# Optimization experiments

Hardware: AMD Instinct MI355X
Metric: run time of the kernel (lower is better)

Reference implementation:

```python
import jax, jax.numpy as jnp
import numpy as np

# dims: batch, seq, d_model, heads, experts, expert hidden, top-k
B, S, D, H, E, F, K = 8, 512, 768, 12, 8, 3072, 2
DH = D // H
TAU = 1.0  # routing temperature
EPS = 1e-5


def _ln(x, g, b):
    mu = jnp.mean(x, axis=-1, keepdims=True)
    var = jnp.var(x, axis=-1, keepdims=True)
    return (x - mu) * jax.lax.rsqrt(var + EPS) * g + b


def setup_inputs() -> dict:
    key = jax.random.key(0)
    ks = jax.random.split(key, 12)
    sd = 1.0 / np.sqrt(D)
    sf = 1.0 / np.sqrt(F)
    return {
        "x": jax.random.normal(ks[0], (B, S, D), jnp.float32),
        "wq": jax.random.normal(ks[1], (D, D), jnp.float32) * sd,
        "wk": jax.random.normal(ks[2], (D, D), jnp.float32) * sd,
        "wv": jax.random.normal(ks[3], (D, D), jnp.float32) * sd,
        "wo": jax.random.normal(ks[4], (D, D), jnp.float32) * sd,
        "ln1_g": jnp.ones((D,), jnp.float32),
        "ln1_b": jnp.zeros((D,), jnp.float32),
        "ln2_g": jnp.ones((D,), jnp.float32),
        "ln2_b": jnp.zeros((D,), jnp.float32),
        "gate_w": jax.random.normal(ks[5], (D, E), jnp.float32) * sd,
        "gate_b": jnp.zeros((E,), jnp.float32),
        "bias_e": jnp.zeros((E,), jnp.float32),  # bias_param: per-expert routing bias (selection only)
        "w1": jax.random.normal(ks[6], (E, D, F), jnp.float32) * sd,
        "b1": jnp.zeros((E, F), jnp.float32),
        "w2": jax.random.normal(ks[7], (E, F, D), jnp.float32) * sf,
        "b2": jnp.zeros((E, D), jnp.float32),
    }


def reference(x, wq, wk, wv, wo, ln1_g, ln1_b, ln2_g, ln2_b,
              gate_w, gate_b, bias_e, w1, b1, w2, b2):
    # --- pre-LN multi-head self-attention + residual ---
    h = _ln(x, ln1_g, ln1_b)
    q = (h @ wq).reshape(B, S, H, DH)
    k = (h @ wk).reshape(B, S, H, DH)
    v = (h @ wv).reshape(B, S, H, DH)
    scores = jnp.einsum("bqhd,bkhd->bhqk", q, k) / np.sqrt(DH).astype(np.float32)
    attn = jax.nn.softmax(scores, axis=-1)
    o = jnp.einsum("bhqk,bkhd->bqhd", attn, v).reshape(B, S, D) @ wo
    x = x + o

    # --- pre-LN top-k MoE + residual ---
    h = _ln(x, ln2_g, ln2_b).reshape(B * S, D)          # [T, D]
    logits = (h @ gate_w + gate_b) / TAU                # [T, E]
    sel_scores = logits + bias_e                        # bias used for selection only
    _, idx = jax.lax.top_k(sel_scores, K)               # [T, K]
    topk_logits = jnp.take_along_axis(logits, idx, axis=-1)
    gates = jax.nn.softmax(topk_logits, axis=-1)        # [T, K]
    # sparse combine weights [T, E]
    cw = jnp.zeros((B * S, E), x.dtype).at[jnp.arange(B * S)[:, None], idx].set(gates)
    mid = jax.nn.gelu(jnp.einsum("td,edf->tef", h, w1) + b1)   # [T, E, F]
    eout = jnp.einsum("tef,efd->ted", mid, w2) + b2            # [T, E, D]
    y = jnp.einsum("ted,te->td", eout, cw).reshape(B, S, D)
    return x + y
```

## Files before the change

kernel.cpp:

```cpp
#include <hip/hip_runtime.h>
#include <hip/hip_bf16.h>

using bf16 = __hip_bfloat16;

constexpr int NB = 8, NS = 512, ND = 768, NH = 12, NE = 8, NF = 3072, NT = 4096;
constexpr int HG = 4;
constexpr int NG = NH / HG;
constexpr int GW = HG * 64;
constexpr int FQ = 768;
constexpr int NP = NF / FQ;

typedef __attribute__((ext_vector_type(8))) short v8s;
typedef __attribute__((ext_vector_type(4))) float v4f;

__device__ __forceinline__ short f2bf(float v) {
    bf16 t = __float2bfloat16(v);
    return *reinterpret_cast<short*>(&t);
}
__device__ __forceinline__ float bf2f(short s) {
    bf16 t = *reinterpret_cast<bf16*>(&s);
    return __bfloat162float(t);
}

template <typename TOUT>
__launch_bounds__(256)
__global__ void ln_kernel(const float* __restrict__ x, const float* __restrict__ g,
                          const float* __restrict__ b, TOUT* __restrict__ out) {
    const int t = blockIdx.x;
    const int tid = threadIdx.x;
    const float* xr = x + (size_t)t * ND;
    float v0 = xr[tid], v1 = xr[tid + 256], v2 = xr[tid + 512];
    float s = v0 + v1 + v2;
    float ss = v0 * v0 + v1 * v1 + v2 * v2;
#pragma unroll
    for (int off = 32; off >= 1; off >>= 1) {
        s += __shfl_xor(s, off);
        ss += __shfl_xor(ss, off);
    }
    __shared__ float rs[4], rss[4];
    const int wv = tid >> 6, ln = tid & 63;
    if (ln == 0) { rs[wv] = s; rss[wv] = ss; }
    __syncthreads();
    float S = rs[0] + rs[1] + rs[2] + rs[3];
    float SS = rss[0] + rss[1] + rss[2] + rss[3];
    float mu = S * (1.0f / ND);
    float var = SS * (1.0f / ND) - mu * mu;
    float r = rsqrtf(fmaxf(var, 0.f) + 1e-5f);
    TOUT* orow = out + (size_t)t * ND;
    float o0 = (v0 - mu) * r * g[tid]       + b[tid];
    float o1 = (v1 - mu) * r * g[tid + 256] + b[tid + 256];
    float o2 = (v2 - mu) * r * g[tid + 512] + b[tid + 512];
    if constexpr (sizeof(TOUT) == 2) {
        orow[tid] = __float2bfloat16(o0);
        orow[tid + 256] = __float2bfloat16(o1);
        orow[tid + 512] = __float2bfloat16(o2);
    } else {
        orow[tid] = o0; orow[tid + 256] = o1; orow[tid + 512] = o2;
    }
}

__device__ __forceinline__ void gemm3_core(const float* __restrict__ A, int lda,
                                           const float* __restrict__ Bsrc, int ldb,
                                           int Kd, int m0, v4f acc[4],
                                           short* Ah, short* Al, short* Bh, short* Bl) {
    const int tid = threadIdx.x, lane = tid & 63, wv = tid >> 6;
    const int qd = lane >> 4, l16 = lane & 15;
    const int ar = tid >> 2, ac = (tid & 3) * 8;
    const int bn = tid & 63, bk = (tid >> 6) * 8;
    const float* Arow = A + (size_t)(m0 + ar) * lda;
    for (int k0 = 0; k0 < Kd; k0 += 32) {
        {
            const float* asrc = Arow + k0 + ac;
            v8s ah, al;
#pragma unroll
            for (int j = 0; j < 8; j++) {
                float vv = asrc[j];
                short hi = f2bf(vv);
                ah[j] = hi;
                al[j] = f2bf(vv - bf2f(hi));
            }
            *(v8s*)&Ah[ar * 40 + ac] = ah;
            *(v8s*)&Al[ar * 40 + ac] = al;
        }
        {
            const float* bsrc = Bsrc + (size_t)(k0 + bk) * ldb + bn;
            v8s bh_, bl_;
#pragma unroll
            for (int j = 0; j < 8; j++) {
                float vv = bsrc[(size_t)j * ldb];
                short hi = f2bf(vv);
                bh_[j] = hi;
                bl_[j] = f2bf(vv - bf2f(hi));
            }
            *(v8s*)&Bh[bn * 40 + bk] = bh_;
            *(v8s*)&Bl[bn * 40 + bk] = bl_;
        }
        __syncthreads();
        v8s bhf = *(const v8s*)&Bh[(wv * 16 + l16) * 40 + qd * 8];
        v8s blf = *(const v8s*)&Bl[(wv * 16 + l16) * 40 + qd * 8];
#pragma unroll
        for (int t = 0; t < 4; t++) {
            v8s ahf = *(const v8s*)&Ah[(t * 16 + l16) * 40 + qd * 8];
            v8s alf = *(const v8s*)&Al[(t * 16 + l16) * 40 + qd * 8];
            acc[t] = __builtin_amdgcn_mfma_f32_16x16x32_bf16(ahf, bhf, acc[t], 0, 0, 0);
            acc[t] = __builtin_amdgcn_mfma_f32_16x16x32_bf16(ahf, blf, acc[t], 0, 0, 0);
            acc[t] = __builtin_amdgcn_mfma_f32_16x16x32_bf16(alf, bhf, acc[t], 0, 0, 0);
        }
        __syncthreads();
    }
}

template <int RES_MODE>
__launch_bounds__(256)
__global__ void sgemm3(const float* __restrict__ A, int lda, const float* __restrict__ Bw,
                       int ldb, int bcol0, const float* __restrict__ Res,
                       float* __restrict__ C, int ldc, int Kd) {
    __shared__ short Ah[64 * 40], Al[64 * 40], Bh[64 * 40], Bl[64 * 40];
    const int m0 = blockIdx.x * 64, n0 = blockIdx.y * 64;
    v4f acc[4] = {};
    gemm3_core(A, lda, Bw + bcol0 + n0, ldb, Kd, m0, acc, Ah, Al, Bh, Bl);
    const int tid = threadIdx.x, lane = tid & 63, wv = tid >> 6;
    const int qd = lane >> 4, l16 = lane & 15;
    const int c = n0 + wv * 16 + l16;
#pragma unroll
    for (int t = 0; t < 4; t++)
#pragma unroll
        for (int rg = 0; rg < 4; rg++) {
            const int r = m0 + t * 16 + qd * 4 + rg;
            size_t ci = (size_t)r * ldc + c;
            if (RES_MODE == 0) C[ci] = acc[t][rg];
            else if (RES_MODE == 1) C[ci] = Res[ci] + acc[t][rg];
            else C[ci] += acc[t][rg];
        }
}

__launch_bounds__(256)
__global__ void qkv3(const float* __restrict__ h, const float* __restrict__ wq,
                     const float* __restrict__ wk, const float* __restrict__ wv,
                     int bcol0, float* __restrict__ qo, float* __restrict__ ko,
                     float* __restrict__ vo) {
    __shared__ short Ah[64 * 40], Al[64 * 40], Bh[64 * 40], Bl[64 * 40];
    const int m0 = blockIdx.x * 64;
    const int ysel = blockIdx.y >> 2, ny = blockIdx.y & 3;
    const int n0 = ny * 64;
    const float* Bw = (ysel == 0) ? wq : (ysel == 1) ? wk : wv;
    float* C = (ysel == 0) ? qo : (ysel == 1) ? ko : vo;
    v4f acc[4] = {};
    gemm3_core(h, ND, Bw + bcol0 + n0, ND, ND, m0, acc, Ah, Al, Bh, Bl);
    const int tid = threadIdx.x, lane = tid & 63, wv_ = tid >> 6;
    const int qd = lane >> 4, l16 = lane & 15;
    const int c = n0 + wv_ * 16 + l16;
#pragma unroll
    for (int t = 0; t < 4; t++)
#pragma unroll
        for (int rg = 0; rg < 4; rg++) {
            const int r = m0 + t * 16 + qd * 4 + rg;
            C[(size_t)r * GW + c] = acc[t][rg];
        }
}

__launch_bounds__(256)
__global__ void attn_kernel(const float* __restrict__ q, const float* __restrict__ k,
                            const float* __restrict__ v, float* __restrict__ o) {
    __shared__ float qs[64][68];
    __shared__ float kp[64][68];
    __shared__ float vs[64][68];
    const int qt = blockIdx.x, hl = blockIdx.y, b = blockIdx.z;
    const int tid = threadIdx.x, tx = tid & 15, ty = tid >> 4;
    const int hc = hl * 64;
    {
        const v4f* q4 = (const v4f*)(q + ((size_t)b * NS + qt * 64) * GW + hc);
#pragma unroll
        for (int i = 0; i < 4; i++) {
            int idx = tid + 256 * i;
            int r = idx >> 4, c4 = idx & 15;
            *(v4f*)&qs[r][c4 * 4] = q4[(size_t)r * (GW / 4) + c4];
        }
    }
    float oa[4][4] = {};
    float mi[4], li[4], al[4];
#pragma unroll
    for (int i = 0; i < 4; i++) { mi[i] = -1.0e30f; li[i] = 0.f; }
    for (int kt = 0; kt < NS / 64; kt++) {
        __syncthreads();
        {
            const v4f* k4 = (const v4f*)(k + ((size_t)b * NS + kt * 64) * GW + hc);
            const v4f* v4 = (const v4f*)(v + ((size_t)b * NS + kt * 64) * GW + hc);
#pragma unroll
            for (int i = 0; i < 4; i++) {
                int idx = tid + 256 * i;
                int r = idx >> 4, c4 = idx & 15;
                *(v4f*)&kp[r][c4 * 4] = k4[(size_t)r * (GW / 4) + c4];
                *(v4f*)&vs[r][c4 * 4] = v4[(size_t)r * (GW / 4) + c4];
            }
        }
        __syncthreads();
        float s[4][4] = {};
#pragma unroll
        for (int d0 = 0; d0 < 64; d0 += 4) {
            v4f av[4], bv[4];
#pragma unroll
            for (int i = 0; i < 4; i++) av[i] = *(const v4f*)&qs[ty + 16 * i][d0];
#pragma unroll
            for (int j = 0; j < 4; j++) bv[j] = *(const v4f*)&kp[tx + 16 * j][d0];
#pragma unroll
            for (int dd = 0; dd < 4; dd++)
#pragma unroll
                for (int i = 0; i < 4; i++)
#pragma unroll
                    for (int j = 0; j < 4; j++) s[i][j] += av[i][dd] * bv[j][dd];
        }
#pragma unroll
        for (int i = 0; i < 4; i++) {
#pragma unroll
            for (int j = 0; j < 4; j++) s[i][j] *= 0.125f;
            float mt = fmaxf(fmaxf(s[i][0], s[i][1]), fmaxf(s[i][2], s[i][3]));
#pragma unroll
            for (int off = 1; off < 16; off <<= 1) mt = fmaxf(mt, __shfl_xor(mt, off));
            float mn = fmaxf(mi[i], mt);
            al[i] = __expf(mi[i] - mn);
            mi[i] = mn;
            float rsum = 0.f;
#pragma unroll
            for (int j = 0; j < 4; j++) {
                s[i][j] = __expf(s[i][j] - mn);
                rsum += s[i][j];
            }
#pragma unroll
            for (int off = 1; off < 16; off <<= 1) rsum += __shfl_xor(rsum, off);
            li[i] = li[i] * al[i] + rsum;
        }
        __syncthreads();
#pragma unroll
        for (int i = 0; i < 4; i++)
#pragma unroll
            for (int j = 0; j < 4; j++) {
                kp[ty + 16 * i][tx + 16 * j] = s[i][j];
                oa[i][j] *= al[i];
            }
        __syncthreads();
#pragma unroll
        for (int d0 = 0; d0 < 64; d0 += 4) {
            v4f av[4];
#pragma unroll
            for (int i = 0; i < 4; i++) av[i] = *(const v4f*)&kp[ty + 16 * i][d0];
#pragma unroll
            for (int dd = 0; dd < 4; dd++) {
                float bb[4];
#pragma unroll
                for (int j = 0; j < 4; j++) bb[j] = vs[d0 + dd][tx + 16 * j];
#pragma unroll
                for (int i = 0; i < 4; i++)
#pragma unroll
                    for (int j = 0; j < 4; j++) oa[i][j] += av[i][dd] * bb[j];
            }
        }
    }
#pragma unroll
    for (int i = 0; i < 4; i++) {
        float inv = 1.0f / li[i];
#pragma unroll
        for (int j = 0; j < 4; j++)
            o[((size_t)b * NS + qt * 64 + ty + 16 * i) * GW + hc + tx + 16 * j] = oa[i][j] * inv;
    }
}

__launch_bounds__(256)
__global__ void route_kernel(const float* __restrict__ x1, const float* __restrict__ lg,
                             const float* __restrict__ lb, const float* __restrict__ gw,
                             const float* __restrict__ gb, const float* __restrict__ be,
                             int* __restrict__ cnt, int* __restrict__ list,
                             float* __restrict__ gates) {
    const int lane = threadIdx.x & 63;
    const int t = blockIdx.x * 4 + (threadIdx.x >> 6);
    if (t >= NT) return;
    const float* xr = x1 + (size_t)t * ND;
    float xv[12];
    float s = 0.f, ss = 0.f;
#pragma unroll
    for (int i = 0; i < 12; i++) {
        xv[i] = xr[i * 64 + lane];
        s += xv[i];
        ss += xv[i] * xv[i];
    }
#pragma unroll
    for (int off = 32; off >= 1; off >>= 1) {
        s += __shfl_xor(s, off);
        ss += __shfl_xor(ss, off);
    }
    float mu = s * (1.0f / ND);
    float var = ss * (1.0f / ND) - mu * mu;
    float r = rsqrtf(fmaxf(var, 0.f) + 1e-5f);
    float le[NE];
#pragma unroll
    for (int e = 0; e < NE; e++) le[e] = 0.f;
#pragma unroll
    for (int i = 0; i < 12; i++) {
        int d = i * 64 + lane;
        float hn = (xv[i] - mu) * r * lg[d] + lb[d];
#pragma unroll
        for (int e = 0; e < NE; e++) le[e] += hn * gw[d * NE + e];
    }
#pragma unroll
    for (int off = 1; off < 64; off <<= 1)
#pragma unroll
        for (int e = 0; e < NE; e++) le[e] += __shfl_xor(le[e], off);
    float sel[NE];
#pragma unroll
    for (int e = 0; e < NE; e++) {
        le[e] += gb[e];
        sel[e] = le[e] + be[e];
    }
    int i1 = 0;
#pragma unroll
    for (int e = 1; e < NE; e++) if (sel[e] > sel[i1]) i1 = e;
    int i2 = (i1 == 0) ? 1 : 0;
#pragma unroll
    for (int e = 0; e < NE; e++) if (e != i1 && sel[e] > sel[i2]) i2 = e;
    float l1 = le[i1], l2 = le[i2];
    float m = fmaxf(l1, l2);
    float e1 = __expf(l1 - m), e2 = __expf(l2 - m);
    float inv = 1.0f / (e1 + e2);
    if (lane == 0) {
        gates[t * 2 + 0] = e1 * inv;
        gates[t * 2 + 1] = e2 * inv;
        int p1 = atomicAdd(&cnt[i1], 1);
        if (p1 < NT) list[i1 * NT + p1] = t * 2 + 0;
        int p2 = atomicAdd(&cnt[i2], 1);
        if (p2 < NT) list[i2 * NT + p2] = t * 2 + 1;
    }
}

__launch_bounds__(256)
__global__ void moe_gemm1(const bf16* __restrict__ h2, const float* __restrict__ w1,
                          const float* __restrict__ b1, const int* __restrict__ cnt,
                          const int* __restrict__ list, bf16* __restrict__ mid, int fcol0) {
    const int e = blockIdx.x >> 6, tile = blockIdx.x & 63;
    const int n = min(cnt[e], NT);
    const int r0 = tile * 64;
    if (r0 >= n) return;
    const int f0 = blockIdx.y * 64;
    __shared__ int ent[64];
    __shared__ short As[64 * 40];
    __shared__ short Bs[64 * 40];
    const int tid = threadIdx.x;
    const int lane = tid & 63, wv = tid >> 6;
    const int qd = lane >> 4, l16 = lane & 15;
    if (tid < 64) {
        int en = (r0 + tid < n) ? list[e * NT + r0 + tid] : -1;
        if (en < 0 || en >= 2 * NT) en = -1;
        ent[tid] = en;
    }
    __syncthreads();
    v4f acc[4] = {};
    const float* w1e = w1 + (size_t)e * ND * NF + fcol0 + f0;
    const int ar = tid >> 2, ac = (tid & 3) * 8;
    const int bn = tid & 63, bk = (tid >> 6) * 8;
    const int aen = ent[ar];
    for (int k0 = 0; k0 < ND; k0 += 32) {
        v8s av = {};
        if (aen >= 0)
            av = *(const v8s*)((const short*)h2 + (size_t)(aen >> 1) * ND + k0 + ac);
        *(v8s*)&As[ar * 40 + ac] = av;
        {
            const float* src = w1e + (size_t)(k0 + bk) * NF + bn;
            v8s bv;
#pragma unroll
            for (int j = 0; j < 8; j++) bv[j] = f2bf(src[(size_t)j * NF]);
            *(v8s*)&Bs[bn * 40 + bk] = bv;
        }
        __syncthreads();
        v8s bfrag = *(const v8s*)&Bs[(wv * 16 + l16) * 40 + qd * 8];
#pragma unroll
        for (int t = 0; t < 4; t++) {
            v8s afrag = *(const v8s*)&As[(t * 16 + l16) * 40 + qd * 8];
            acc[t] = __builtin_amdgcn_mfma_f32_16x16x32_bf16(afrag, bfrag, acc[t], 0, 0, 0);
        }
        __syncthreads();
    }
    const int col = wv * 16 + l16;
    const float bias = b1[e * NF + fcol0 + f0 + col];
#pragma unroll
    for (int t = 0; t < 4; t++) {
#pragma unroll
        for (int rg = 0; rg < 4; rg++) {
            int en = ent[t * 16 + qd * 4 + rg];
            if (en < 0) continue;
            float xv = acc[t][rg] + bias;
            float th = tanhf(0.7978845608028654f * (xv + 0.044715f * xv * xv * xv));
            mid[((size_t)((en & 1) * NT) + (en >> 1)) * FQ + f0 + col] =
                __float2bfloat16(0.5f * xv * (1.0f + th));
        }
    }
}

__launch_bounds__(256)
__global__ void moe_gemm2(const bf16* __restrict__ mid, const float* __restrict__ w2,
                          const float* __restrict__ b2, const int* __restrict__ cnt,
                          const int* __restrict__ list, const float* __restrict__ gates,
                          float* __restrict__ x1, int fcol0, int add_b2) {
    const int e = blockIdx.x >> 6, tile = blockIdx.x & 63;
    const int n = min(cnt[e], NT);
    const int r0 = tile * 64;
    if (r0 >= n) return;
    const int d0 = blockIdx.y * 64;
    __shared__ int ent[64];
    __shared__ short As[64 * 40];
    __shared__ short Bs[64 * 40];
    const int tid = threadIdx.x;
    const int lane = tid & 63, wv = tid >> 6;
    const int qd = lane >> 4, l16 = lane & 15;
    if (tid < 64) {
        int en = (r0 + tid < n) ? list[e * NT + r0 + tid] : -1;
        if (en < 0 || en >= 2 * NT) en = -1;
        ent[tid] = en;
    }
    __syncthreads();
    v4f acc[4] = {};
    const float* w2e = w2 + (size_t)e * NF * ND + d0;
    const int ar = tid >> 2, ac = (tid & 3) * 8;
    const int bn = tid & 63, bk = (tid >> 6) * 8;
    const int aen = ent[ar];
    for (int k0 = 0; k0 < FQ; k0 += 32) {
        v8s av = {};
        if (aen >= 0)
            av = *(const v8s*)((const short*)mid +
                               ((size_t)((aen & 1) * NT) + (aen >> 1)) * FQ + k0 + ac);
        *(v8s*)&As[ar * 40 + ac] = av;
        {
            const float* src = w2e + (size_t)(fcol0 + k0 + bk) * ND + bn;
            v8s bv;
#pragma unroll
            for (int j = 0; j < 8; j++) bv[j] = f2bf(src[(size_t)j * ND]);
            *(v8s*)&Bs[bn * 40 + bk] = bv;
        }
        __syncthreads();
        v8s bfrag = *(const v8s*)&Bs[(wv * 16 + l16) * 40 + qd * 8];
#pragma unroll
        for (int t = 0; t < 4; t++) {
            v8s afrag = *(const v8s*)&As[(t * 16 + l16) * 40 + qd * 8];
            acc[t] = __builtin_amdgcn_mfma_f32_16x16x32_bf16(afrag, bfrag, acc[t], 0, 0, 0);
        }
        __syncthreads();
    }
    const int col = wv * 16 + l16;
    const float bias = add_b2 ? b2[e * ND + d0 + col] : 0.f;
#pragma unroll
    for (int t = 0; t < 4; t++) {
#pragma unroll
        for (int rg = 0; rg < 4; rg++) {
            int en = ent[t * 16 + qd * 4 + rg];
            if (en < 0) continue;
            float g = gates[en];
            atomicAdd(&x1[(size_t)(en >> 1) * ND + d0 + col], g * (acc[t][rg] + bias));
        }
    }
}

__launch_bounds__(256)
__global__ void final_kernel(const float* __restrict__ x1, float* __restrict__ out) {
    int i = blockIdx.x * 256 + threadIdx.x;
    out[i] = x1[i];
}

extern "C" void kernel_launch(void* const* d_in, const int* in_sizes, int n_in,
                              void* d_out, int out_size, void* d_ws, size_t ws_size,
                              hipStream_t stream) {
    const float* x    = (const float*)d_in[0];
    const float* wq   = (const float*)d_in[1];
    const float* wk   = (const float*)d_in[2];
    const float* wvp  = (const float*)d_in[3];
    const float* wo   = (const float*)d_in[4];
    const float* ln1g = (const float*)d_in[5];
    const float* ln1b = (const float*)d_in[6];
    const float* ln2g = (const float*)d_in[7];
    const float* ln2b = (const float*)d_in[8];
    const float* gw   = (const float*)d_in[9];
    const float* gb   = (const float*)d_in[10];
    const float* be   = (const float*)d_in[11];
    const float* w1   = (const float*)d_in[12];
    const float* b1   = (const float*)d_in[13];
    const float* w2   = (const float*)d_in[14];
    const float* b2   = (const float*)d_in[15];
    float* out = (float*)d_out;

    const size_t TDn = (size_t)NT * ND;
    const size_t TGn = (size_t)NT * GW;
    float* W = (float*)d_ws;
    int*   cnt   = (int*)W;
    int*   list  = cnt + NE;
    float* gates = (float*)(list + NE * NT);
    float* x1 = W + 41216;
    float* h  = x1 + TDn;
    float* R0 = h + TDn;
    float* q  = R0;
    float* k  = R0 + TGn;
    float* v  = R0 + 2 * TGn;
    float* og = R0 + 3 * TGn;
    bf16*  h2  = (bf16*)h;
    bf16*  mid = (bf16*)R0;

    hipMemsetAsync(cnt, 0, NE * sizeof(int), stream);

    ln_kernel<float><<<NT, 256, 0, stream>>>(x, ln1g, ln1b, h);
    for (int g = 0; g < NG; g++) {
        qkv3<<<dim3(NT / 64, 12), 256, 0, stream>>>(h, wq, wk, wvp, g * GW, q, k, v);
        attn_kernel<<<dim3(NS / 64, HG, NB), 256, 0, stream>>>(q, k, v, og);
        if (g == 0)
            sgemm3<1><<<dim3(NT / 64, ND / 64), 256, 0, stream>>>(
                og, GW, wo + (size_t)g * GW * ND, ND, 0, x, x1, ND, GW);
        else
            sgemm3<2><<<dim3(NT / 64, ND / 64), 256, 0, stream>>>(
                og, GW, wo + (size_t)g * GW * ND, ND, 0, nullptr, x1, ND, GW);
    }
    route_kernel<<<NT / 4, 256, 0, stream>>>(x1, ln2g, ln2b, gw, gb, be, cnt, list, gates);
    ln_kernel<bf16><<<NT, 256, 0, stream>>>(x1, ln2g, ln2b, h2);
    for (int p = 0; p < NP; p++) {
        int fcol0 = p * FQ;
        moe_gemm1<<<dim3(NE * (NT / 64), FQ / 64), 256, 0, stream>>>(
            h2, w1, b1, cnt, list, mid, fcol0);
        moe_gemm2<<<dim3(NE * (NT / 64), ND / 64), 256, 0, stream>>>(
            mid, w2, b2, cnt, list, gates, x1, fcol0, p == 0 ? 1 : 0);
    }
    final_kernel<<<TDn / 256, 256, 0, stream>>>(x1, out);
}
```

Baseline: 1.211 ms.

## Fuse second layernorm into routing kernel and widen attention blocks to 512 threads

After: 1.198 ms. About the same (-1.1%).

```diff
diff --git a/kernel.cpp b/kernel.cpp
--- a/kernel.cpp
+++ b/kernel.cpp
@@ -22,10 +22,9 @@
     return __bfloat162float(t);
 }
 
-template <typename TOUT>
 __launch_bounds__(256)
 __global__ void ln_kernel(const float* __restrict__ x, const float* __restrict__ g,
-                          const float* __restrict__ b, TOUT* __restrict__ out) {
+                          const float* __restrict__ b, float* __restrict__ out) {
     const int t = blockIdx.x;
     const int tid = threadIdx.x;
     const float* xr = x + (size_t)t * ND;
@@ -46,17 +45,10 @@
     float mu = S * (1.0f / ND);
     float var = SS * (1.0f / ND) - mu * mu;
     float r = rsqrtf(fmaxf(var, 0.f) + 1e-5f);
-    TOUT* orow = out + (size_t)t * ND;
-    float o0 = (v0 - mu) * r * g[tid]       + b[tid];
-    float o1 = (v1 - mu) * r * g[tid + 256] + b[tid + 256];
-    float o2 = (v2 - mu) * r * g[tid + 512] + b[tid + 512];
-    if constexpr (sizeof(TOUT) == 2) {
-        orow[tid] = __float2bfloat16(o0);
-        orow[tid + 256] = __float2bfloat16(o1);
-        orow[tid + 512] = __float2bfloat16(o2);
-    } else {
-        orow[tid] = o0; orow[tid + 256] = o1; orow[tid + 512] = o2;
-    }
+    float* orow = out + (size_t)t * ND;
+    orow[tid]       = (v0 - mu) * r * g[tid]       + b[tid];
+    orow[tid + 256] = (v1 - mu) * r * g[tid + 256] + b[tid + 256];
+    orow[tid + 512] = (v2 - mu) * r * g[tid + 512] + b[tid + 512];
 }
 
 __device__ __forceinline__ void gemm3_core(const float* __restrict__ A, int lda,
@@ -159,59 +151,62 @@
         }
 }
 
-__launch_bounds__(256)
+__launch_bounds__(512)
 __global__ void attn_kernel(const float* __restrict__ q, const float* __restrict__ k,
                             const float* __restrict__ v, float* __restrict__ o) {
     __shared__ float qs[64][68];
     __shared__ float kp[64][68];
     __shared__ float vs[64][68];
     const int qt = blockIdx.x, hl = blockIdx.y, b = blockIdx.z;
-    const int tid = threadIdx.x, tx = tid & 15, ty = tid >> 4;
+    const int tid = threadIdx.x;
+    const int half = tid >> 8, t8 = tid & 255;
+    const int tx = t8 & 15, ty = t8 >> 4;
     const int hc = hl * 64;
+    const int rb = half * 32 + ty;
     {
         const v4f* q4 = (const v4f*)(q + ((size_t)b * NS + qt * 64) * GW + hc);
 #pragma unroll
-        for (int i = 0; i < 4; i++) {
-            int idx = tid + 256 * i;
+        for (int i = 0; i < 2; i++) {
+            int idx = tid + 512 * i;
             int r = idx >> 4, c4 = idx & 15;
             *(v4f*)&qs[r][c4 * 4] = q4[(size_t)r * (GW / 4) + c4];
         }
     }
-    float oa[4][4] = {};
-    float mi[4], li[4], al[4];
-#pragma unroll
-    for (int i = 0; i < 4; i++) { mi[i] = -1.0e30f; li[i] = 0.f; }
+    float oa[2][4] = {};
+    float mi[2], li[2], al[2];
+#pragma unroll
+    for (int i = 0; i < 2; i++) { mi[i] = -1.0e30f; li[i] = 0.f; }
     for (int kt = 0; kt < NS / 64; kt++) {
         __syncthreads();
         {
             const v4f* k4 = (const v4f*)(k + ((size_t)b * NS + kt * 64) * GW + hc);
             const v4f* v4 = (const v4f*)(v + ((size_t)b * NS + kt * 64) * GW + hc);
 #pragma unroll
-            for (int i = 0; i < 4; i++) {
-                int idx = tid + 256 * i;
+            for (int i = 0; i < 2; i++) {
+                int idx = tid + 512 * i;
                 int r = idx >> 4, c4 = idx & 15;
                 *(v4f*)&kp[r][c4 * 4] = k4[(size_t)r * (GW / 4) + c4];
                 *(v4f*)&vs[r][c4 * 4] = v4[(size_t)r * (GW / 4) + c4];
             }
         }
         __syncthreads();
-        float s[4][4] = {};
+        float s[2][4] = {};
 #pragma unroll
         for (int d0 = 0; d0 < 64; d0 += 4) {
-            v4f av[4], bv[4];
-#pragma unroll
-            for (int i = 0; i < 4; i++) av[i] = *(const v4f*)&qs[ty + 16 * i][d0];
+            v4f av[2], bv[4];
+#pragma unroll
+            for (int i = 0; i < 2; i++) av[i] = *(const v4f*)&qs[rb + 16 * i][d0];
 #pragma unroll
             for (int j = 0; j < 4; j++) bv[j] = *(const v4f*)&kp[tx + 16 * j][d0];
 #pragma unroll
             for (int dd = 0; dd < 4; dd++)
 #pragma unroll
-                for (int i = 0; i < 4; i++)
+                for (int i = 0; i < 2; i++)
 #pragma unroll
                     for (int j = 0; j < 4; j++) s[i][j] += av[i][dd] * bv[j][dd];
         }
 #pragma unroll
-        for (int i = 0; i < 4; i++) {
+        for (int i = 0; i < 2; i++) {
 #pragma unroll
             for (int j = 0; j < 4; j++) s[i][j] *= 0.125f;
             float mt = fmaxf(fmaxf(s[i][0], s[i][1]), fmaxf(s[i][2], s[i][3]));
@@ -232,36 +227,36 @@
         }
         __syncthreads();
 #pragma unroll
-        for (int i = 0; i < 4; i++)
+        for (int i = 0; i < 2; i++)
 #pragma unroll
             for (int j = 0; j < 4; j++) {
-                kp[ty + 16 * i][tx + 16 * j] = s[i][j];
+                kp[rb + 16 * i][tx + 16 * j] = s[i][j];
                 oa[i][j] *= al[i];
             }
         __syncthreads();
 #pragma unroll
         for (int d0 = 0; d0 < 64; d0 += 4) {
-            v4f av[4];
-#pragma unroll
-            for (int i = 0; i < 4; i++) av[i] = *(const v4f*)&kp[ty + 16 * i][d0];
+            v4f av[2];
+#pragma unroll
+            for (int i = 0; i < 2; i++) av[i] = *(const v4f*)&kp[rb + 16 * i][d0];
 #pragma unroll
             for (int dd = 0; dd < 4; dd++) {
                 float bb[4];
 #pragma unroll
                 for (int j = 0; j < 4; j++) bb[j] = vs[d0 + dd][tx + 16 * j];
 #pragma unroll
-                for (int i = 0; i < 4; i++)
+                for (int i = 0; i < 2; i++)
 #pragma unroll
                     for (int j = 0; j < 4; j++) oa[i][j] += av[i][dd] * bb[j];
             }
         }
     }
 #pragma unroll
-    for (int i = 0; i < 4; i++) {
+    for (int i = 0; i < 2; i++) {
         float inv = 1.0f / li[i];
 #pragma unroll
         for (int j = 0; j < 4; j++)
-            o[((size_t)b * NS + qt * 64 + ty + 16 * i) * GW + hc + tx + 16 * j] = oa[i][j] * inv;
+            o[((size_t)b * NS + qt * 64 + rb + 16 * i) * GW + hc + tx + 16 * j] = oa[i][j] * inv;
     }
 }
 
@@ -270,7 +265,7 @@
                              const float* __restrict__ lb, const float* __restrict__ gw,
                              const float* __restrict__ gb, const float* __restrict__ be,
                              int* __restrict__ cnt, int* __restrict__ list,
-                             float* __restrict__ gates) {
+                             float* __restrict__ gates, bf16* __restrict__ h2) {
     const int lane = threadIdx.x & 63;
     const int t = blockIdx.x * 4 + (threadIdx.x >> 6);
     if (t >= NT) return;
@@ -294,10 +289,12 @@
     float le[NE];
 #pragma unroll
     for (int e = 0; e < NE; e++) le[e] = 0.f;
+    bf16* h2r = h2 + (size_t)t * ND;
 #pragma unroll
     for (int i = 0; i < 12; i++) {
         int d = i * 64 + lane;
         float hn = (xv[i] - mu) * r * lg[d] + lb[d];
+        h2r[d] = __float2bfloat16(hn);
 #pragma unroll
         for (int e = 0; e < NE; e++) le[e] += hn * gw[d * NE + e];
     }
@@ -305,19 +302,20 @@
     for (int off = 1; off < 64; off <<= 1)
 #pragma unroll
         for (int e = 0; e < NE; e++) le[e] += __shfl_xor(le[e], off);
-    float sel[NE];
+    float m1 = -1.0e30f, m2 = -1.0e30f, l1 = 0.f, l2 = 0.f;
+    int i1 = 0, i2 = 0;
 #pragma unroll
     for (int e = 0; e < NE; e++) {
-        le[e] += gb[e];
-        sel[e] = le[e] + be[e];
-    }
-    int i1 = 0;
-#pragma unroll
-    for (int e = 1; e < NE; e++) if (sel[e] > sel[i1]) i1 = e;
-    int i2 = (i1 == 0) ? 1 : 0;
-#pragma unroll
-    for (int e = 0; e < NE; e++) if (e != i1 && sel[e] > sel[i2]) i2 = e;
-    float l1 = le[i1], l2 = le[i2];
+        float lv = le[e] + gb[e];
+        float sv = lv + be[e];
+        bool g1 = sv > m1;
+        float pm1 = m1, pl1 = l1; int pi1 = i1;
+        m1 = g1 ? sv : m1; l1 = g1 ? lv : l1; i1 = g1 ? e : i1;
+        bool g2 = (!g1) && (sv > m2);
+        m2 = g1 ? pm1 : (g2 ? sv : m2);
+        l2 = g1 ? pl1 : (g2 ? lv : l2);
+        i2 = g1 ? pi1 : (g2 ? e : i2);
+    }
     float m = fmaxf(l1, l2);
     float e1 = __expf(l1 - m), e2 = __expf(l2 - m);
     float inv = 1.0f / (e1 + e2);
@@ -502,10 +500,10 @@
 
     hipMemsetAsync(cnt, 0, NE * sizeof(int), stream);
 
-    ln_kernel<float><<<NT, 256, 0, stream>>>(x, ln1g, ln1b, h);
+    ln_kernel<<<NT, 256, 0, stream>>>(x, ln1g, ln1b, h);
     for (int g = 0; g < NG; g++) {
         qkv3<<<dim3(NT / 64, 12), 256, 0, stream>>>(h, wq, wk, wvp, g * GW, q, k, v);
-        attn_kernel<<<dim3(NS / 64, HG, NB), 256, 0, stream>>>(q, k, v, og);
+        attn_kernel<<<dim3(NS / 64, HG, NB), 512, 0, stream>>>(q, k, v, og);
         if (g == 0)
             sgemm3<1><<<dim3(NT / 64, ND / 64), 256, 0, stream>>>(
                 og, GW, wo + (size_t)g * GW * ND, ND, 0, x, x1, ND, GW);
@@ -513,8 +511,8 @@
             sgemm3<2><<<dim3(NT / 64, ND / 64), 256, 0, stream>>>(
                 og, GW, wo + (size_t)g * GW * ND, ND, 0, nullptr, x1, ND, GW);
     }
-    route_kernel<<<NT / 4, 256, 0, stream>>>(x1, ln2g, ln2b, gw, gb, be, cnt, list, gates);
-    ln_kernel<bf16><<<NT, 256, 0, stream>>>(x1, ln2g, ln2b, h2);
+    route_kernel<<<NT / 4, 256, 0, stream>>>(x1, ln2g, ln2b, gw, gb, be, cnt, list,
+                                             gates, h2);
     for (int p = 0; p < NP; p++) {
         int fcol0 = p * FQ;
         moe_gemm1<<<dim3(NE * (NT / 64), FQ / 64), 256, 0, stream>>>(
```
